# Kernel optimization log

Hardware: AMD Instinct MI355X
Metric: run time of the kernel (lower is better)

## Reference

```python
import jax, jax.numpy as jnp
import numpy as np

LN_EPS = 1e-5  # torch nn.LayerNorm default
L2_EPS = 1e-12  # F.normalize default


def layer_norm(x, gamma, beta):
    mu = jnp.mean(x, axis=-1, keepdims=True)
    var = jnp.mean(jnp.square(x - mu), axis=-1, keepdims=True)
    return (x - mu) * jax.lax.rsqrt(var + LN_EPS) * gamma + beta


def l2_normalize(x):
    n = jnp.linalg.norm(x, axis=-1, keepdims=True)
    return x / jnp.maximum(n, L2_EPS)


def setup_inputs() -> dict:
    key = jax.random.key(0)
    k_x, k_mu = jax.random.split(key, 2)
    B, C, H, W = 4, 512, 128, 128
    K, M = 19, 5  # num_classes, num_components_per_class
    x = jax.random.normal(k_x, (B, C, H, W), dtype=jnp.float32)
    means = 0.02 * jax.random.normal(k_mu, (K, M, C), dtype=jnp.float32)  # trunc_normal_(std=0.02)
    diagonal = jnp.ones((K, M, C), dtype=jnp.float32)
    feat_gamma = jnp.ones((C,), dtype=jnp.float32)
    feat_beta = jnp.zeros((C,), dtype=jnp.float32)
    mask_gamma = jnp.ones((K,), dtype=jnp.float32)
    mask_beta = jnp.zeros((K,), dtype=jnp.float32)
    return dict(x=x, means=means, diagonal=diagonal,
                feat_gamma=feat_gamma, feat_beta=feat_beta,
                mask_gamma=mask_gamma, mask_beta=mask_beta)


def reference(x, means, diagonal, feat_gamma, feat_beta, mask_gamma, mask_beta):
    B, C, H, W = x.shape
    K, M, D = means.shape
    # rearrange 'b c h w -> (b h w) c'
    f = jnp.transpose(x, (0, 2, 3, 1)).reshape(-1, C)  # (N, D)
    f = layer_norm(f, feat_gamma, feat_beta)
    f = l2_normalize(f)
    # means are re-normalized in-place each forward
    mu = l2_normalize(means).reshape(K * M, D)          # (P, D), P = K*M
    sigma = diagonal.reshape(K * M, D)                  # diagonal scale (std)
    inv_var = 1.0 / jnp.square(sigma)
    # Mahalanobis distance via quadratic expansion (avoids (N,P,D) intermediate):
    # sum_d ((f - mu)/sigma)^2 = f^2 . iv - 2 f . (mu*iv) + sum(mu^2 * iv)
    q1 = jnp.square(f) @ inv_var.T                      # (N, P)
    q2 = f @ (mu * inv_var).T                           # (N, P)
    q3 = jnp.sum(jnp.square(mu) * inv_var, axis=-1)     # (P,)
    maha = q1 - 2.0 * q2 + q3[None, :]
    log_det = jnp.sum(jnp.log(sigma), axis=-1)          # sum log sigma, (P,)
    half_log2pi = 0.5 * D * jnp.log(2.0 * jnp.pi)
    log_prob = -0.5 * maha - log_det[None, :] - half_log2pi  # (N, P)
    log_prob = log_prob.reshape(-1, K, M)
    m_prob = jnp.max(log_prob, axis=-1)                 # amax over components, (N, K)
    out = layer_norm(m_prob, mask_gamma, mask_beta)
    # rearrange '(b h w) k -> b k h w'
    out_seg = jnp.transpose(out.reshape(B, H, W, K), (0, 3, 1, 2))
    return out_seg
```

## Files before the change

kernel.cpp:

```cpp
#include <hip/hip_runtime.h>
#include <math.h>

#define C_ 512
#define HW_ 16384
#define K_ 19
#define M_ 5
#define P_ 95
#define P2 96
#define TPX 32
#define NBLK 2048
#define HL2PI 470.49652900081467f

typedef __attribute__((ext_vector_type(8))) short short8;
typedef __attribute__((ext_vector_type(4))) int int4v;
typedef __attribute__((ext_vector_type(4))) float float4v;

static __device__ __forceinline__ short f2bf(float f) {
  unsigned u = __builtin_bit_cast(unsigned, f);
  unsigned r = (u + 0x7fffu + ((u >> 16) & 1u)) >> 16;
  return (short)r;
}

static __device__ __forceinline__ int pk2(float a, float b) {
  int r;
  asm("v_cvt_pk_bf16_f32 %0, %1, %2" : "=v"(r) : "v"(a), "v"(b));
  return r;
}

static __device__ __forceinline__ short8 sq8(short8 a) {
  int4v ai = __builtin_bit_cast(int4v, a);
  int4v ri;
#pragma unroll
  for (int j = 0; j < 4; j++) {
    unsigned u = (unsigned)ai[j];
    float lo = __builtin_bit_cast(float, u << 16);
    float hi = __builtin_bit_cast(float, u & 0xffff0000u);
    ri[j] = pk2(lo * lo, hi * hi);
  }
  return __builtin_bit_cast(short8, ri);
}

__device__ __forceinline__ float block_reduce_sum(float v, volatile float* red) {
#pragma unroll
  for (int o = 32; o; o >>= 1) v += __shfl_down(v, o);
  const int lane = threadIdx.x & 63, wv = threadIdx.x >> 6;
  if (lane == 0) red[wv] = v;
  __syncthreads();
  float r = red[0] + red[1] + red[2] + red[3];
  __syncthreads();
  return r;
}

__global__ __launch_bounds__(256) void prep_kernel(
    const float* __restrict__ means, const float* __restrict__ diag,
    short* __restrict__ wbf, float* __restrict__ cterm) {
  const int p = blockIdx.x;
  const int tid = threadIdx.x;
  __shared__ float red[4];
  if (p >= P_) {
    for (int c = tid; c < C_; c += 256) {
      wbf[p * 1024 + c] = 0;
      wbf[p * 1024 + 512 + c] = 0;
    }
    if (tid == 0) cterm[p] = 0.f;
    return;
  }
  const float* mrow = means + (size_t)p * C_;
  const float* srow = diag + (size_t)p * C_;
  float m0 = mrow[tid], m1 = mrow[tid + 256];
  float ss = block_reduce_sum(m0 * m0 + m1 * m1, red);
  float rden = 1.f / fmaxf(sqrtf(ss), 1e-12f);
  float q3 = 0.f, ld = 0.f;
#pragma unroll
  for (int t = 0; t < 2; t++) {
    int c = tid + t * 256;
    float m = mrow[c], s = srow[c];
    float mu = m * rden;
    float iv = 1.f / (s * s);
    wbf[p * 1024 + c] = f2bf(iv);
    wbf[p * 1024 + 512 + c] = f2bf(mu * iv);
    q3 += mu * mu * iv;
    ld += logf(s);
  }
  q3 = block_reduce_sum(q3, red);
  ld = block_reduce_sum(ld, red);
  if (tid == 0) cterm[p] = -0.5f * q3 - ld - HL2PI;
}

__global__ __launch_bounds__(256) void main_kernel(
    const float* __restrict__ x,
    const float* __restrict__ fg, const float* __restrict__ fb,
    const float* __restrict__ mg, const float* __restrict__ mb,
    const short* __restrict__ wbf, const float* __restrict__ cterm,
    float* __restrict__ out) {
  __shared__ __align__(16) char raw[16384];
  __shared__ float red1[256];
  __shared__ float meanA[TPX], rstdA[TPX], rnA[TPX], rn2A[TPX];
  __shared__ float mean2A[TPX], rstd2A[TPX];

  const int tid = threadIdx.x;
  const int px = tid & 31, part = tid >> 5;
  const int wv = tid >> 6, lane = tid & 63;
  const int n0 = blockIdx.x * TPX;
  const int b = n0 >> 14;
  const int rem = n0 & 16383;
  const int h = rem >> 7;
  const int w0 = rem & 127;
  const int t_ = px >> 4, lq = px & 15;
  const float* xp = x + (size_t)b * C_ * HW_ + h * 128 + w0 + px;

  float* red0 = (float*)raw;
  {
    float s = 0.f, q = 0.f;
#pragma unroll 1
    for (int g = 0; g < 8; g++) {
      float xv[8];
#pragma unroll
      for (int j = 0; j < 8; j++) xv[j] = xp[(size_t)(part * 64 + g * 8 + j) * HW_];
#pragma unroll
      for (int j = 0; j < 8; j++) {
        s += xv[j];
        q = fmaf(xv[j], xv[j], q);
      }
    }
    red0[tid] = s;
    red1[tid] = q;
  }
  __syncthreads();
  if (tid < 32) {
    float ss = 0.f, qq = 0.f;
#pragma unroll
    for (int i = 0; i < 8; i++) {
      ss += red0[i * 32 + tid];
      qq += red1[i * 32 + tid];
    }
    float mean = ss * (1.f / C_);
    float var = qq * (1.f / C_) - mean * mean;
    meanA[tid] = mean;
    rstdA[tid] = rsqrtf(var + 1e-5f);
  }
  __syncthreads();

  const int pbase = (wv & 1) * 3;
  const int khalf = wv >> 1;
  const int lm = lane & 15, lk = lane >> 4;
  float4v acc[3][2] = {{}, {}, {}};
  const short* wrow = wbf + (((pbase * 16 + lm) << 10) + (khalf << 9) + (lk << 3));
  float s2 = 0.f;
  const float mean = meanA[px], rstd = rstdA[px];

#pragma unroll 1
  for (int half = 0; half < 2; half++) {
#pragma unroll
    for (int j8 = 0; j8 < 4; j8++) {
      const int c0 = half * 256 + part * 32 + j8 * 8;
      float xv[8];
#pragma unroll
      for (int j = 0; j < 8; j++) xv[j] = xp[(size_t)(c0 + j) * HW_];
      float vv[8];
#pragma unroll
      for (int j = 0; j < 8; j++) {
        float v = fmaf((xv[j] - mean) * rstd, fg[c0 + j], fb[c0 + j]);
        s2 = fmaf(v, v, s2);
        vv[j] = v;
      }
      int4v pk;
#pragma unroll
      for (int j2 = 0; j2 < 4; j2++) pk[j2] = pk2(vv[2 * j2], vv[2 * j2 + 1]);
      const int ksl = (c0 >> 5) & 7;
      *(int4v*)(raw + (((t_ * 8 + ksl) << 10) | (((c0 >> 3) & 3) << 8) | (lq << 4))) = pk;
    }
    __syncthreads();

#pragma unroll 4
    for (int ksl = 0; ksl < 8; ksl++) {
      const int kk = half * 8 + ksl;
      short8 a0 = *(const short8*)(wrow + kk * 32);
      short8 a1 = *(const short8*)(wrow + 16384 + kk * 32);
      short8 a2 = *(const short8*)(wrow + 32768 + kk * 32);
      short8 b0 = *(const short8*)(raw + ((ksl << 10) | (lane << 4)));
      short8 b1 = *(const short8*)(raw + (((8 + ksl) << 10) | (lane << 4)));
      if (khalf == 0) {
        b0 = sq8(b0);
        b1 = sq8(b1);
      }
      acc[0][0] = __builtin_amdgcn_mfma_f32_16x16x32_bf16(a0, b0, acc[0][0], 0, 0, 0);
      acc[0][1] = __builtin_amdgcn_mfma_f32_16x16x32_bf16(a0, b1, acc[0][1], 0, 0, 0);
      acc[1][0] = __builtin_amdgcn_mfma_f32_16x16x32_bf16(a1, b0, acc[1][0], 0, 0, 0);
      acc[1][1] = __builtin_amdgcn_mfma_f32_16x16x32_bf16(a1, b1, acc[1][1], 0, 0, 0);
      acc[2][0] = __builtin_amdgcn_mfma_f32_16x16x32_bf16(a2, b0, acc[2][0], 0, 0, 0);
      acc[2][1] = __builtin_amdgcn_mfma_f32_16x16x32_bf16(a2, b1, acc[2][1], 0, 0, 0);
    }
    __syncthreads();
  }

  red1[tid] = s2;
  __syncthreads();
  if (tid < 32) {
    float ss = 0.f;
#pragma unroll
    for (int i = 0; i < 8; i++) ss += red1[i * 32 + tid];
    float rn = 1.f / fmaxf(sqrtf(ss), 1e-12f);
    rnA[tid] = rn;
    rn2A[tid] = rn * rn;
  }
  __syncthreads();

  float* lp = (float*)raw;
  float* mpr = (float*)(raw + 12800);

  if (khalf == 0) {
#pragma unroll
    for (int i = 0; i < 3; i++) {
      const int prow = (pbase + i) * 16 + lk * 4;
#pragma unroll
      for (int r = 0; r < 4; r++) {
        const float ct = cterm[prow + r];
#pragma unroll
        for (int t2 = 0; t2 < 2; t2++) {
          const int pxx = t2 * 16 + lm;
          lp[pxx * 100 + prow + r] = fmaf(-0.5f * rn2A[pxx], acc[i][t2][r], ct);
        }
      }
    }
  }
  __syncthreads();
  if (khalf == 1) {
#pragma unroll
    for (int i = 0; i < 3; i++) {
      const int prow = (pbase + i) * 16 + lk * 4;
#pragma unroll
      for (int r = 0; r < 4; r++) {
#pragma unroll
        for (int t2 = 0; t2 < 2; t2++) {
          const int pxx = t2 * 16 + lm;
          lp[pxx * 100 + prow + r] += rnA[pxx] * acc[i][t2][r];
        }
      }
    }
  }
  __syncthreads();

  for (int idx = tid; idx < TPX * K_; idx += 256) {
    const int pxx = idx / K_;
    const int k = idx - pxx * K_;
    const float* row = lp + pxx * 100 + k * M_;
    float mv = row[0];
#pragma unroll
    for (int m = 1; m < M_; m++) mv = fmaxf(mv, row[m]);
    mpr[pxx * 20 + k] = mv;
  }
  __syncthreads();
  if (tid < 32) {
    float ss = 0.f;
    for (int k = 0; k < K_; k++) ss += mpr[tid * 20 + k];
    float m2 = ss * (1.f / K_);
    float qq = 0.f;
    for (int k = 0; k < K_; k++) {
      float d = mpr[tid * 20 + k] - m2;
      qq += d * d;
    }
    mean2A[tid] = m2;
    rstd2A[tid] = rsqrtf(qq * (1.f / K_) + 1e-5f);
  }
  __syncthreads();
  float* obase = out + ((size_t)(b * K_) * 128 + h) * 128 + w0;
  for (int idx = tid; idx < TPX * K_; idx += 256) {
    const int k = idx >> 5, pxx = idx & 31;
    float v = fmaf((mpr[pxx * 20 + k] - mean2A[pxx]) * rstd2A[pxx], mg[k], mb[k]);
    obase[(size_t)k * HW_ + pxx] = v;
  }
}

extern "C" void kernel_launch(void* const* d_in, const int* in_sizes, int n_in,
                              void* d_out, int out_size, void* d_ws, size_t ws_size,
                              hipStream_t stream) {
  const float* x = (const float*)d_in[0];
  const float* means = (const float*)d_in[1];
  const float* diag = (const float*)d_in[2];
  const float* fg = (const float*)d_in[3];
  const float* fb = (const float*)d_in[4];
  const float* mg = (const float*)d_in[5];
  const float* mb = (const float*)d_in[6];
  float* out = (float*)d_out;

  short* wbf = (short*)d_ws;
  float* cterm = (float*)((char*)d_ws + (size_t)P2 * 1024 * 2);

  prep_kernel<<<P2, 256, 0, stream>>>(means, diag, wbf, cterm);
  main_kernel<<<NBLK, 256, 0, stream>>>(x, fg, fb, mg, mb, wbf, cterm, out);
}
```

Baseline: 81.10 us.

## Read input once via float4 loads, stage bf16 copy in LDS for normalization

Each thread now loads four adjacent pixels with 16-byte vector loads instead of scalar strided loads. The raw x tile is stored once as bf16 in a 32 KB shared buffer, so the LayerNorm pass reads it back from LDS rather than reading x from global memory a second time. Statistics are reduced with wave shuffles, and the whole 512-channel tile is staged before a single 16-step MFMA loop. This removes the second global read and gives wider loads. In exchange it doubles shared memory per block, which may lower occupancy, and it computes the normalization from bf16-rounded inputs, which adds precision error.

```diff
diff --git a/kernel.cpp b/kernel.cpp
--- a/kernel.cpp
+++ b/kernel.cpp
@@ -19,6 +19,9 @@
   unsigned u = __builtin_bit_cast(unsigned, f);
   unsigned r = (u + 0x7fffu + ((u >> 16) & 1u)) >> 16;
   return (short)r;
+}
+static __device__ __forceinline__ float bf2f(short s) {
+  return __builtin_bit_cast(float, ((unsigned)(unsigned short)s) << 16);
 }
 
 static __device__ __forceinline__ int pk2(float a, float b) {
@@ -93,46 +96,64 @@
     const float* __restrict__ mg, const float* __restrict__ mb,
     const short* __restrict__ wbf, const float* __restrict__ cterm,
     float* __restrict__ out) {
-  __shared__ __align__(16) char raw[16384];
-  __shared__ float red1[256];
+  __shared__ __align__(16) char raw[32768];
+  __shared__ float redS[128], redQ[128];
   __shared__ float meanA[TPX], rstdA[TPX], rnA[TPX], rn2A[TPX];
   __shared__ float mean2A[TPX], rstd2A[TPX];
+  __shared__ float mpr[TPX * 20];
 
   const int tid = threadIdx.x;
-  const int px = tid & 31, part = tid >> 5;
   const int wv = tid >> 6, lane = tid & 63;
+  const int cg = tid >> 3, q = tid & 7;
   const int n0 = blockIdx.x * TPX;
   const int b = n0 >> 14;
   const int rem = n0 & 16383;
   const int h = rem >> 7;
   const int w0 = rem & 127;
-  const int t_ = px >> 4, lq = px & 15;
-  const float* xp = x + (size_t)b * C_ * HW_ + h * 128 + w0 + px;
-
-  float* red0 = (float*)raw;
-  {
-    float s = 0.f, q = 0.f;
-#pragma unroll 1
-    for (int g = 0; g < 8; g++) {
-      float xv[8];
-#pragma unroll
-      for (int j = 0; j < 8; j++) xv[j] = xp[(size_t)(part * 64 + g * 8 + j) * HW_];
-#pragma unroll
-      for (int j = 0; j < 8; j++) {
-        s += xv[j];
-        q = fmaf(xv[j], xv[j], q);
-      }
-    }
-    red0[tid] = s;
-    red1[tid] = q;
+  const int c16 = cg * 16;
+  const int blkw = (q >> 2) * 16 + (cg >> 1);
+  const int sbase = (q & 3) * 2 + (cg & 1);
+  const float* xp4 = x + (size_t)b * C_ * HW_ + h * 128 + w0 + q * 4;
+
+  float4v s4 = {0.f, 0.f, 0.f, 0.f}, q4 = {0.f, 0.f, 0.f, 0.f};
+#pragma unroll
+  for (int hc = 0; hc < 2; hc++) {
+    float4v xq[8];
+#pragma unroll
+    for (int i = 0; i < 8; i++)
+      xq[i] = *(const float4v*)(xp4 + (size_t)(c16 + hc * 8 + i) * HW_);
+#pragma unroll
+    for (int i = 0; i < 8; i++) {
+      s4 += xq[i];
+      q4 += xq[i] * xq[i];
+    }
+#pragma unroll
+    for (int r = 0; r < 4; r++) {
+      int4v pk;
+#pragma unroll
+      for (int j2 = 0; j2 < 4; j2++) pk[j2] = pk2(xq[2 * j2][r], xq[2 * j2 + 1][r]);
+      *(int4v*)(raw + blkw * 1024 + ((hc * 4 + r) * 8 + sbase) * 16) = pk;
+    }
+  }
+#pragma unroll
+  for (int o = 8; o < 64; o <<= 1) {
+#pragma unroll
+    for (int c = 0; c < 4; c++) {
+      s4[c] += __shfl_down(s4[c], o);
+      q4[c] += __shfl_down(q4[c], o);
+    }
+  }
+  if (lane < 8) {
+    *(float4v*)(redS + (wv * 8 + lane) * 4) = s4;
+    *(float4v*)(redQ + (wv * 8 + lane) * 4) = q4;
   }
   __syncthreads();
   if (tid < 32) {
     float ss = 0.f, qq = 0.f;
 #pragma unroll
-    for (int i = 0; i < 8; i++) {
-      ss += red0[i * 32 + tid];
-      qq += red1[i * 32 + tid];
+    for (int w = 0; w < 4; w++) {
+      ss += redS[(w * 8 + (tid >> 2)) * 4 + (tid & 3)];
+      qq += redQ[(w * 8 + (tid >> 2)) * 4 + (tid & 3)];
     }
     float mean = ss * (1.f / C_);
     float var = qq * (1.f / C_) - mean * mean;
@@ -141,73 +162,81 @@
   }
   __syncthreads();
 
+  {
+    float fga[16], fba[16];
+#pragma unroll
+    for (int i = 0; i < 4; i++) {
+      *(float4v*)(fga + i * 4) = *(const float4v*)(fg + c16 + i * 4);
+      *(float4v*)(fba + i * 4) = *(const float4v*)(fb + c16 + i * 4);
+    }
+    const float4v mean4 = *(const float4v*)(meanA + q * 4);
+    const float4v rstd4 = *(const float4v*)(rstdA + q * 4);
+    float4v s2 = {0.f, 0.f, 0.f, 0.f};
+#pragma unroll
+    for (int hc = 0; hc < 2; hc++) {
+#pragma unroll
+      for (int r = 0; r < 4; r++) {
+        char* ad = raw + blkw * 1024 + ((hc * 4 + r) * 8 + sbase) * 16;
+        short8 xc = *(short8*)ad;
+        const float m = mean4[r], sd = rstd4[r];
+        float vv[8];
+#pragma unroll
+        for (int j = 0; j < 8; j++) {
+          float v = fmaf((bf2f(xc[j]) - m) * sd, fga[hc * 8 + j], fba[hc * 8 + j]);
+          s2[r] = fmaf(v, v, s2[r]);
+          vv[j] = v;
+        }
+        int4v pk;
+#pragma unroll
+        for (int j2 = 0; j2 < 4; j2++) pk[j2] = pk2(vv[2 * j2], vv[2 * j2 + 1]);
+        *(int4v*)ad = pk;
+      }
+    }
+#pragma unroll
+    for (int o = 8; o < 64; o <<= 1) {
+#pragma unroll
+      for (int c = 0; c < 4; c++) s2[c] += __shfl_down(s2[c], o);
+    }
+    if (lane < 8) *(float4v*)(redS + (wv * 8 + lane) * 4) = s2;
+  }
+  __syncthreads();
+  if (tid < 32) {
+    float ss = 0.f;
+#pragma unroll
+    for (int w = 0; w < 4; w++) ss += redS[(w * 8 + (tid >> 2)) * 4 + (tid & 3)];
+    float rn = 1.f / fmaxf(sqrtf(ss), 1e-12f);
+    rnA[tid] = rn;
+    rn2A[tid] = rn * rn;
+  }
+  __syncthreads();
+
   const int pbase = (wv & 1) * 3;
   const int khalf = wv >> 1;
   const int lm = lane & 15, lk = lane >> 4;
+  const int slotR =
+      ((((lane >> 4) & 1) * 4 + (lane & 3)) * 8 + ((lane >> 2) & 3) * 2 + ((lane >> 5) & 1)) * 16;
   float4v acc[3][2] = {{}, {}, {}};
   const short* wrow = wbf + (((pbase * 16 + lm) << 10) + (khalf << 9) + (lk << 3));
-  float s2 = 0.f;
-  const float mean = meanA[px], rstd = rstdA[px];
-
-#pragma unroll 1
-  for (int half = 0; half < 2; half++) {
-#pragma unroll
-    for (int j8 = 0; j8 < 4; j8++) {
-      const int c0 = half * 256 + part * 32 + j8 * 8;
-      float xv[8];
-#pragma unroll
-      for (int j = 0; j < 8; j++) xv[j] = xp[(size_t)(c0 + j) * HW_];
-      float vv[8];
-#pragma unroll
-      for (int j = 0; j < 8; j++) {
-        float v = fmaf((xv[j] - mean) * rstd, fg[c0 + j], fb[c0 + j]);
-        s2 = fmaf(v, v, s2);
-        vv[j] = v;
-      }
-      int4v pk;
-#pragma unroll
-      for (int j2 = 0; j2 < 4; j2++) pk[j2] = pk2(vv[2 * j2], vv[2 * j2 + 1]);
-      const int ksl = (c0 >> 5) & 7;
-      *(int4v*)(raw + (((t_ * 8 + ksl) << 10) | (((c0 >> 3) & 3) << 8) | (lq << 4))) = pk;
-    }
-    __syncthreads();
-
 #pragma unroll 4
-    for (int ksl = 0; ksl < 8; ksl++) {
-      const int kk = half * 8 + ksl;
-      short8 a0 = *(const short8*)(wrow + kk * 32);
-      short8 a1 = *(const short8*)(wrow + 16384 + kk * 32);
-      short8 a2 = *(const short8*)(wrow + 32768 + kk * 32);
-      short8 b0 = *(const short8*)(raw + ((ksl << 10) | (lane << 4)));
-      short8 b1 = *(const short8*)(raw + (((8 + ksl) << 10) | (lane << 4)));
-      if (khalf == 0) {
-        b0 = sq8(b0);
-        b1 = sq8(b1);
-      }
-      acc[0][0] = __builtin_amdgcn_mfma_f32_16x16x32_bf16(a0, b0, acc[0][0], 0, 0, 0);
-      acc[0][1] = __builtin_amdgcn_mfma_f32_16x16x32_bf16(a0, b1, acc[0][1], 0, 0, 0);
-      acc[1][0] = __builtin_amdgcn_mfma_f32_16x16x32_bf16(a1, b0, acc[1][0], 0, 0, 0);
-      acc[1][1] = __builtin_amdgcn_mfma_f32_16x16x32_bf16(a1, b1, acc[1][1], 0, 0, 0);
-      acc[2][0] = __builtin_amdgcn_mfma_f32_16x16x32_bf16(a2, b0, acc[2][0], 0, 0, 0);
-      acc[2][1] = __builtin_amdgcn_mfma_f32_16x16x32_bf16(a2, b1, acc[2][1], 0, 0, 0);
-    }
-    __syncthreads();
-  }
-
-  red1[tid] = s2;
-  __syncthreads();
-  if (tid < 32) {
-    float ss = 0.f;
-#pragma unroll
-    for (int i = 0; i < 8; i++) ss += red1[i * 32 + tid];
-    float rn = 1.f / fmaxf(sqrtf(ss), 1e-12f);
-    rnA[tid] = rn;
-    rn2A[tid] = rn * rn;
-  }
-  __syncthreads();
-
+  for (int ksl = 0; ksl < 16; ksl++) {
+    short8 a0 = *(const short8*)(wrow + ksl * 32);
+    short8 a1 = *(const short8*)(wrow + 16384 + ksl * 32);
+    short8 a2 = *(const short8*)(wrow + 32768 + ksl * 32);
+    short8 b0 = *(const short8*)(raw + ksl * 1024 + slotR);
+    short8 b1 = *(const short8*)(raw + (16 + ksl) * 1024 + slotR);
+    if (khalf == 0) {
+      b0 = sq8(b0);
+      b1 = sq8(b1);
+    }
+    acc[0][0] = __builtin_amdgcn_mfma_f32_16x16x32_bf16(a0, b0, acc[0][0], 0, 0, 0);
+    acc[0][1] = __builtin_amdgcn_mfma_f32_16x16x32_bf16(a0, b1, acc[0][1], 0, 0, 0);
+    acc[1][0] = __builtin_amdgcn_mfma_f32_16x16x32_bf16(a1, b0, acc[1][0], 0, 0, 0);
+    acc[1][1] = __builtin_amdgcn_mfma_f32_16x16x32_bf16(a1, b1, acc[1][1], 0, 0, 0);
+    acc[2][0] = __builtin_amdgcn_mfma_f32_16x16x32_bf16(a2, b0, acc[2][0], 0, 0, 0);
+    acc[2][1] = __builtin_amdgcn_mfma_f32_16x16x32_bf16(a2, b1, acc[2][1], 0, 0, 0);
+  }
+  __syncthreads();
   float* lp = (float*)raw;
-  float* mpr = (float*)(raw + 12800);
 
   if (khalf == 0) {
 #pragma unroll
```

Measured after the change: 69.44 us. 14.4% less time.
